# Performance work log

Hardware: AMD Instinct MI355X
Metric: run time of the kernel (lower is better)

The kernel has to match this reference:

```python
import jax, jax.numpy as jnp
import numpy as np

D = 1024
H = 16
K = 32768
EPS = 1e-5


def setup_inputs() -> dict:
    key = jax.random.key(0)
    ks = jax.random.split(key, 12)
    s = 1.0 / np.sqrt(D)
    return {
        "query": jax.random.normal(ks[0], (D,), jnp.float32),
        "neighbors": jax.random.normal(ks[1], (K, D), jnp.float32),
        # nn.MultiheadAttention params
        "in_proj_w": jax.random.uniform(ks[2], (3 * D, D), jnp.float32, -s, s),
        "in_proj_b": jnp.zeros((3 * D,), jnp.float32),
        "out_proj_w": jax.random.uniform(ks[3], (D, D), jnp.float32, -s, s),
        "out_proj_b": jnp.zeros((D,), jnp.float32),
        # FFN params
        "w1": jax.random.uniform(ks[4], (4 * D, D), jnp.float32, -s, s),
        "b1": jnp.zeros((4 * D,), jnp.float32),
        "w2": jax.random.uniform(ks[5], (D, 4 * D), jnp.float32, -s, s),
        "b2": jnp.zeros((D,), jnp.float32),
        # LayerNorm params
        "g1": jnp.ones((D,), jnp.float32),
        "be1": jnp.zeros((D,), jnp.float32),
        "g2": jnp.ones((D,), jnp.float32),
        "be2": jnp.zeros((D,), jnp.float32),
    }


def _layernorm(x, g, b):
    m = jnp.mean(x, axis=-1, keepdims=True)
    v = jnp.var(x, axis=-1, keepdims=True)
    return (x - m) * jax.lax.rsqrt(v + EPS) * g + b


def reference(query, neighbors, in_proj_w, in_proj_b, out_proj_w, out_proj_b,
              w1, b1, w2, b2, g1, be1, g2, be2):
    dh = D // H
    wq, wk, wv = in_proj_w[:D], in_proj_w[D:2 * D], in_proj_w[2 * D:]
    bq, bk, bv = in_proj_b[:D], in_proj_b[D:2 * D], in_proj_b[2 * D:]

    q = (query @ wq.T + bq).reshape(H, dh)            # [H, dh]
    k = (neighbors @ wk.T + bk).reshape(K, H, dh)     # [K, H, dh]
    v = (neighbors @ wv.T + bv).reshape(K, H, dh)

    scores = jnp.einsum('hd,khd->hk', q, k) / np.sqrt(dh)  # [H, K]
    attn = jax.nn.softmax(scores, axis=-1)
    ctx = jnp.einsum('hk,khd->hd', attn, v).reshape(D)      # [D]
    attn_out = ctx @ out_proj_w.T + out_proj_b

    x = _layernorm(query + attn_out, g1, be1)
    ffn = jax.nn.gelu(x @ w1.T + b1, approximate=False) @ w2.T + b2
    return _layernorm(x + ffn, g2, be2)
```

## Files before the change

kernel.cpp:

```cpp
#include <hip/hip_runtime.h>
#include <hip/hip_bf16.h>

#define D 1024
#define H 16
#define DH 64
#define KN 32768
#define EPS 1e-5f

__device__ __forceinline__ float wave_sum(float v){
  #pragma unroll
  for (int off = 32; off; off >>= 1) v += __shfl_xor(v, off, 64);
  return v;
}

#define GLL(gp, lp) __builtin_amdgcn_global_load_lds((const __attribute__((address_space(1))) void*)(gp), (__attribute__((address_space(3))) void*)(lp), 16, 0, 0)

__global__ __launch_bounds__(256) void g_qk(const float* __restrict__ query,
                                            const float* __restrict__ ipw, const float* __restrict__ ipb,
                                            float* __restrict__ qk, float* __restrict__ sb){
  int b = blockIdx.x, t = threadIdx.x;
  int h = b >> 2, sl = b & 3;
  int w = t >> 6, ci = t & 63;
  __shared__ float qh[DH];
  __shared__ float4 red[256];

  {
    const float4* qv = (const float4*)(query + ci*16);
    #pragma unroll 1
    for (int jj = 0; jj < 16; jj += 2){
      int j0 = h*DH + w*16 + jj;
      const float4* w0 = (const float4*)(ipw + (size_t)j0*D + ci*16);
      const float4* w1r = (const float4*)(ipw + (size_t)(j0+1)*D + ci*16);
      float a0 = 0.f, a1 = 0.f;
      #pragma unroll
      for (int c = 0; c < 4; c++){
        float4 qq = qv[c];
        float4 x0 = w0[c];
        float4 x1 = w1r[c];
        a0 += x0.x*qq.x + x0.y*qq.y + x0.z*qq.z + x0.w*qq.w;
        a1 += x1.x*qq.x + x1.y*qq.y + x1.z*qq.z + x1.w*qq.w;
      }
      a0 = wave_sum(a0);
      a1 = wave_sum(a1);
      if (ci == 0){
        qh[w*16 + jj]     = a0 + ipb[j0];
        qh[w*16 + jj + 1] = a1 + ipb[j0 + 1];
      }
    }
  }
  __syncthreads();

  if (t < DH){
    float p = qh[t] * ipb[D + h*DH + t];
    p = wave_sum(p);
    if (t == 0 && sl == 0) sb[h] = p;
  }
  float4 acc = make_float4(0.f,0.f,0.f,0.f);
  for (int jj = 0; jj < 16; jj++){
    int j = w*16 + jj;
    float4 ww = *((const float4*)(ipw + (size_t)(D + h*DH + j)*D) + sl*64 + ci);
    float qj = qh[j];
    acc.x += qj*ww.x; acc.y += qj*ww.y; acc.z += qj*ww.z; acc.w += qj*ww.w;
  }
  red[t] = acc;
  __syncthreads();
  if (w == 0){
    float4 a = red[ci], b1 = red[64+ci], c1 = red[128+ci], d1 = red[192+ci];
    float4 r = make_float4(a.x+b1.x+c1.x+d1.x, a.y+b1.y+c1.y+d1.y,
                           a.z+b1.z+c1.z+d1.z, a.w+b1.w+c1.w+d1.w);
    ((float4*)(qk + h*D))[sl*64 + ci] = r;
  }
}

__device__ __forceinline__ float bf4(float s0, float s1, float s2, float s3, int ci){
  const bool lo32 = (ci & 32) == 0;
  float za = lo32 ? s2 : s0;
  float ka = lo32 ? s0 : s2;
  float u02 = ka + __shfl_xor(za, 32, 64);
  float zb = lo32 ? s3 : s1;
  float kb = lo32 ? s1 : s3;
  float u13 = kb + __shfl_xor(zb, 32, 64);
  const bool lo16 = (ci & 16) == 0;
  float zc = lo16 ? u13 : u02;
  float kc = lo16 ? u02 : u13;
  float v = kc + __shfl_xor(zc, 16, 64);
  v += __shfl_xor(v, 8, 64);
  v += __shfl_xor(v, 4, 64);
  v += __shfl_xor(v, 2, 64);
  v += __shfl_xor(v, 1, 64);
  return v;
}

__global__ __launch_bounds__(256, 2) void g_attn(const float* __restrict__ nbr, const float* __restrict__ qk,
                       const float* __restrict__ sb, float* __restrict__ lpart,
                       float* __restrict__ part, int rows_per_blk){
  __shared__ __align__(16) float tile[2][8*D];
  const int t = threadIdx.x;
  const int w = t >> 6, ci = t & 63;
  const int wb = t & ~63;
  const int g = (ci >> 4) & 3;
  const float sbl = sb[w*4 + g];

  float qk0[16], qk1[16], qk2[16], qk3[16];
  {
    const float4* p0 = (const float4*)(qk + (w*4+0)*D);
    const float4* p1 = (const float4*)(qk + (w*4+1)*D);
    const float4* p2 = (const float4*)(qk + (w*4+2)*D);
    const float4* p3 = (const float4*)(qk + (w*4+3)*D);
    #pragma unroll
    for (int c = 0; c < 4; c++){
      float4 f;
      f = p0[c*64 + ci]; qk0[4*c]=f.x; qk0[4*c+1]=f.y; qk0[4*c+2]=f.z; qk0[4*c+3]=f.w;
      f = p1[c*64 + ci]; qk1[4*c]=f.x; qk1[4*c+1]=f.y; qk1[4*c+2]=f.z; qk1[4*c+3]=f.w;
      f = p2[c*64 + ci]; qk2[4*c]=f.x; qk2[4*c+1]=f.y; qk2[4*c+2]=f.z; qk2[4*c+3]=f.w;
      f = p3[c*64 + ci]; qk3[4*c]=f.x; qk3[4*c+1]=f.y; qk3[4*c+2]=f.z; qk3[4*c+3]=f.w;
    }
  }
  float acc0[16], acc1[16], acc2[16], acc3[16];
  #pragma unroll
  for (int i = 0; i < 16; i++){ acc0[i]=0.f; acc1[i]=0.f; acc2[i]=0.f; acc3[i]=0.f; }
  float lsum = 0.f;

  const int k0 = blockIdx.x * rows_per_blk;
  const int ntiles = rows_per_blk >> 3;
  const uint4* gb = (const uint4*)nbr;

  {
    const uint4* gsrc = gb + (size_t)k0*256;
    #pragma unroll
    for (int i = 0; i < 8; i++) GLL(gsrc + i*256 + t, &tile[0][(i*256 + wb)*4]);
  }
  __syncthreads();

  #pragma unroll 1
  for (int tl = 0; tl < ntiles; tl++){
    int cur = tl & 1;
    if (tl + 1 < ntiles){
      const uint4* gsrc = gb + (size_t)(k0 + (tl+1)*8)*256;
      #pragma unroll
      for (int i = 0; i < 8; i++) GLL(gsrc + i*256 + t, &tile[cur^1][(i*256 + wb)*4]);
    }
    __builtin_amdgcn_s_setprio(1);
    #pragma unroll 1
    for (int r = 0; r < 8; r += 2){
      const float4* rowA = (const float4*)(tile[cur]) + r*256;
      float xfA[16], xfB[16];
      float sA0=0.f,sA1=0.f,sA2=0.f,sA3=0.f;
      float sB0=0.f,sB1=0.f,sB2=0.f,sB3=0.f;
      #pragma unroll
      for (int c = 0; c < 4; c++){
        float4 a = rowA[c*64 + ci];
        xfA[4*c]=a.x; xfA[4*c+1]=a.y; xfA[4*c+2]=a.z; xfA[4*c+3]=a.w;
        sA0 += a.x*qk0[4*c] + a.y*qk0[4*c+1] + a.z*qk0[4*c+2] + a.w*qk0[4*c+3];
        sA1 += a.x*qk1[4*c] + a.y*qk1[4*c+1] + a.z*qk1[4*c+2] + a.w*qk1[4*c+3];
        sA2 += a.x*qk2[4*c] + a.y*qk2[4*c+1] + a.z*qk2[4*c+2] + a.w*qk2[4*c+3];
        sA3 += a.x*qk3[4*c] + a.y*qk3[4*c+1] + a.z*qk3[4*c+2] + a.w*qk3[4*c+3];
      }
      #pragma unroll
      for (int c = 0; c < 4; c++){
        float4 a = rowA[256 + c*64 + ci];
        xfB[4*c]=a.x; xfB[4*c+1]=a.y; xfB[4*c+2]=a.z; xfB[4*c+3]=a.w;
        sB0 += a.x*qk0[4*c] + a.y*qk0[4*c+1] + a.z*qk0[4*c+2] + a.w*qk0[4*c+3];
        sB1 += a.x*qk1[4*c] + a.y*qk1[4*c+1] + a.z*qk1[4*c+2] + a.w*qk1[4*c+3];
        sB2 += a.x*qk2[4*c] + a.y*qk2[4*c+1] + a.z*qk2[4*c+2] + a.w*qk2[4*c+3];
        sB3 += a.x*qk3[4*c] + a.y*qk3[4*c+1] + a.z*qk3[4*c+2] + a.w*qk3[4*c+3];
      }
      float vA = bf4(sA0, sA1, sA2, sA3, ci);
      float vB = bf4(sB0, sB1, sB2, sB3, ci);
      float pA = __expf((vA + sbl)*0.125f);
      float pB = __expf((vB + sbl)*0.125f);
      lsum += pA + pB;
      float pA0 = __shfl(pA, 0, 64), pA1 = __shfl(pA, 16, 64);
      float pA2 = __shfl(pA, 32, 64), pA3 = __shfl(pA, 48, 64);
      float pB0 = __shfl(pB, 0, 64), pB1 = __shfl(pB, 16, 64);
      float pB2 = __shfl(pB, 32, 64), pB3 = __shfl(pB, 48, 64);
      #pragma unroll
      for (int j = 0; j < 16; j++){
        acc0[j] += pA0*xfA[j] + pB0*xfB[j];
        acc1[j] += pA1*xfA[j] + pB1*xfB[j];
        acc2[j] += pA2*xfA[j] + pB2*xfB[j];
        acc3[j] += pA3*xfA[j] + pB3*xfB[j];
      }
    }
    __builtin_amdgcn_s_setprio(0);
    __syncthreads();
  }

  if ((ci & 15) == 0) lpart[blockIdx.x*H + w*4 + g] = lsum;
  float4* o = (float4*)(part + (size_t)blockIdx.x*(H*D) + (size_t)(w*4)*D);
  #pragma unroll
  for (int c = 0; c < 4; c++){
    o[0*256 + c*64 + ci] = make_float4(acc0[4*c], acc0[4*c+1], acc0[4*c+2], acc0[4*c+3]);
    o[1*256 + c*64 + ci] = make_float4(acc1[4*c], acc1[4*c+1], acc1[4*c+2], acc1[4*c+3]);
    o[2*256 + c*64 + ci] = make_float4(acc2[4*c], acc2[4*c+1], acc2[4*c+2], acc2[4*c+3]);
    o[3*256 + c*64 + ci] = make_float4(acc3[4*c], acc3[4*c+1], acc3[4*c+2], acc3[4*c+3]);
  }
}

__global__ __launch_bounds__(1024) void g_red(const float* __restrict__ part, const float* __restrict__ lpart,
                                              float* __restrict__ nb, float* __restrict__ lh, int nblk){
  int b = blockIdx.x, t = threadIdx.x;
  __shared__ float red[1024];
  if (b == 256){
    if (t < 256){
      int hh = t & 15, cs = t >> 4, per = nblk >> 4;
      float s = 0.f;
      for (int k = 0; k < per; k++) s += lpart[(cs*per + k)*H + hh];
      red[t] = s;
    }
    __syncthreads();
    if (t < 16){
      float a = 0.f;
      #pragma unroll
      for (int i = 0; i < 16; i++) a += red[i*16 + t];
      lh[t] = a;
    }
    return;
  }
  int o0 = b * 64;
  int oo = t & 63, cs = t >> 6;
  int per = nblk >> 4;
  float s = 0.f;
  #pragma unroll 8
  for (int k = 0; k < per; k++) s += part[(size_t)(cs*per + k)*(H*D) + o0 + oo];
  red[t] = s;
  __syncthreads();
  if (t < 64){
    float a = 0.f;
    #pragma unroll
    for (int i = 0; i < 16; i++) a += red[i*64 + t];
    nb[o0 + t] = a;
  }
}

__global__ void g_ctx(const float* __restrict__ ipw, const float* __restrict__ ipb,
                      const float* __restrict__ nb, const float* __restrict__ lh,
                      float* __restrict__ ctx){
  int j = blockIdx.x, l = threadIdx.x, h = j >> 6;
  const float4* wv = (const float4*)(ipw + (size_t)(2*D + j)*D + l*16);
  const float4* nv = (const float4*)(nb + h*D + l*16);
  float acc = 0.f;
  #pragma unroll
  for (int t = 0; t < 4; t++){
    float4 b = wv[t], n = nv[t];
    acc += b.x*n.x + b.y*n.y + b.z*n.z + b.w*n.w;
  }
  acc = wave_sum(acc);
  if (l == 0) ctx[j] = acc/lh[h] + ipb[2*D + j];
}

__global__ void g_attnout(const float* __restrict__ opw, const float* __restrict__ opb,
                          const float* __restrict__ query, const float* __restrict__ ctx,
                          float* __restrict__ xb){
  int j = blockIdx.x, l = threadIdx.x;
  const float4* wv = (const float4*)(opw + (size_t)j*D + l*16);
  const float4* cv = (const float4*)(ctx + l*16);
  float acc = 0.f;
  #pragma unroll
  for (int t = 0; t < 4; t++){
    float4 b = wv[t], c = cv[t];
    acc += b.x*c.x + b.y*c.y + b.z*c.z + b.w*c.w;
  }
  acc = wave_sum(acc);
  if (l == 0) xb[j] = query[j] + acc + opb[j];
}

__global__ __launch_bounds__(256) void g_ffn1(const float* __restrict__ w1, const float* __restrict__ b1,
                                              const float* __restrict__ xb,
                                              const float* __restrict__ g1, const float* __restrict__ be1,
                                              float* __restrict__ xln, float* __restrict__ h1){
  int t = threadIdx.x, b = blockIdx.x;
  __shared__ float xs[D];
  __shared__ float red[8];
  float4 v = ((const float4*)xb)[t];
  float s = wave_sum(v.x + v.y + v.z + v.w);
  if ((t & 63) == 0) red[t >> 6] = s;
  __syncthreads();
  float m = (red[0]+red[1]+red[2]+red[3]) * (1.0f/D);
  float4 d = make_float4(v.x-m, v.y-m, v.z-m, v.w-m);
  float s2 = wave_sum(d.x*d.x + d.y*d.y + d.z*d.z + d.w*d.w);
  if ((t & 63) == 0) red[4 + (t >> 6)] = s2;
  __syncthreads();
  float var = (red[4]+red[5]+red[6]+red[7]) * (1.0f/D);
  float rs = rsqrtf(var + EPS);
  float4 gg = ((const float4*)g1)[t], bb = ((const float4*)be1)[t];
  float4 r = make_float4(d.x*rs*gg.x + bb.x, d.y*rs*gg.y + bb.y,
                         d.z*rs*gg.z + bb.z, d.w*rs*gg.w + bb.w);
  ((float4*)xs)[t] = r;
  if (b == 0) ((float4*)xln)[t] = r;
  __syncthreads();

  int w = t >> 6, l = t & 63;
  const float4* xs4 = (const float4*)xs;
  #pragma unroll 1
  for (int rr = 0; rr < 4; rr++){
    int j = b*16 + w*4 + rr;
    const float4* wr = (const float4*)(w1 + (size_t)j*D);
    float a = 0.f;
    #pragma unroll
    for (int c = 0; c < 4; c++){
      float4 ww = wr[c*64 + l], xx = xs4[c*64 + l];
      a += ww.x*xx.x + ww.y*xx.y + ww.z*xx.z + ww.w*xx.w;
    }
    a = wave_sum(a);
    if (l == 0){
      float z = a + b1[j];
      h1[j] = 0.5f*z*(1.0f + erff(z*0.70710678118654752f));
    }
  }
}

__global__ void g_ffn2(const float* __restrict__ w2, const float* __restrict__ b2v,
                       const float* __restrict__ h1, float* __restrict__ y){
  int j = blockIdx.x, l = threadIdx.x;
  const float4* wv = (const float4*)(w2 + (size_t)j*4096 + l*64);
  const float4* hv = (const float4*)(h1 + l*64);
  float acc = 0.f;
  #pragma unroll
  for (int t = 0; t < 16; t++){
    float4 b = wv[t], hh = hv[t];
    acc += b.x*hh.x + b.y*hh.y + b.z*hh.z + b.w*hh.w;
  }
  acc = wave_sum(acc);
  if (l == 0) y[j] = acc + b2v[j];
}

__global__ __launch_bounds__(1024) void g_ln2(const float* __restrict__ xln, const float* __restrict__ y,
                                              const float* __restrict__ g, const float* __restrict__ be,
                                              float* __restrict__ out){
  int t = threadIdx.x;
  __shared__ float red[16];
  __shared__ float bc;
  float v = xln[t] + y[t];
  float s = wave_sum(v);
  if ((t & 63) == 0) red[t >> 6] = s;
  __syncthreads();
  if (t == 0){ float a = 0.f; for (int i = 0; i < 16; i++) a += red[i]; bc = a*(1.0f/D); }
  __syncthreads();
  float m = bc;
  float d = v - m;
  float s2 = wave_sum(d*d);
  if ((t & 63) == 0) red[t >> 6] = s2;
  __syncthreads();
  if (t == 0){ float a = 0.f; for (int i = 0; i < 16; i++) a += red[i]; bc = a*(1.0f/D); }
  __syncthreads();
  float rs = rsqrtf(bc + EPS);
  out[t] = d*rs*g[t] + be[t];
}

extern "C" void kernel_launch(void* const* d_in, const int* in_sizes, int n_in,
                              void* d_out, int out_size, void* d_ws, size_t ws_size,
                              hipStream_t stream) {
  const float* query = (const float*)d_in[0];
  const float* nbr   = (const float*)d_in[1];
  const float* ipw   = (const float*)d_in[2];
  const float* ipb   = (const float*)d_in[3];
  const float* opw   = (const float*)d_in[4];
  const float* opb   = (const float*)d_in[5];
  const float* w1    = (const float*)d_in[6];
  const float* b1    = (const float*)d_in[7];
  const float* w2    = (const float*)d_in[8];
  const float* b2v   = (const float*)d_in[9];
  const float* g1    = (const float*)d_in[10];
  const float* be1   = (const float*)d_in[11];
  const float* g2    = (const float*)d_in[12];
  const float* be2   = (const float*)d_in[13];

  float* ws    = (float*)d_ws;
  float* qk    = ws;
  float* sb    = qk + H*D;
  float* lh    = sb + 16;
  float* ctx   = lh + 16;
  float* xb    = ctx + D;
  float* xln   = xb + D;
  float* h1    = xln + D;
  float* y     = h1 + 4*D;
  float* nb    = y + D;
  float* lpart = nb + H*D;
  float* part  = lpart + 8192;

  size_t fixed_bytes = (size_t)(part - ws) * 4;
  int nblk = 512;
  while (nblk > 64 && fixed_bytes + (size_t)nblk*H*D*4 > ws_size) nblk >>= 1;
  int rows_per_blk = KN / nblk;

  g_qk     <<<64, 256, 0, stream>>>(query, ipw, ipb, qk, sb);
  g_attn   <<<nblk, 256, 0, stream>>>(nbr, qk, sb, lpart, part, rows_per_blk);
  g_red    <<<257, 1024, 0, stream>>>(part, lpart, nb, lh, nblk);
  g_ctx    <<<1024, 64, 0, stream>>>(ipw, ipb, nb, lh, ctx);
  g_attnout<<<1024, 64, 0, stream>>>(opw, opb, query, ctx, xb);
  g_ffn1   <<<256, 256, 0, stream>>>(w1, b1, xb, g1, be1, xln, h1);
  g_ffn2   <<<1024, 64, 0, stream>>>(w2, b2v, h1, y);
  g_ln2    <<<1, 1024, 0, stream>>>(xln, y, g2, be2, (float*)d_out);
}
```

Measured before the change: 306.9 us.

## Split attention heads across 8 waves and coalesce FFN2 weight loads

The attention kernel now launches 512 threads per block, so each wave handles 2 heads instead of 4. This halves the per-thread qk and accumulator register arrays and removes the two-row batching and the priority hints, with the aim of raising occupancy for latency hiding. The LDS tile load is spread across the 512 threads. Separately, the FFN2 kernel now reads weights and activations with a stride across lanes so the loads coalesce, instead of each lane reading a contiguous 64-float chunk. The risk is that the neighbor tile in LDS is now read by 8 waves instead of 4, doubling LDS read traffic per row.

```diff
diff --git a/kernel.cpp b/kernel.cpp
--- a/kernel.cpp
+++ b/kernel.cpp
@@ -72,53 +72,30 @@
   }
 }
 
-__device__ __forceinline__ float bf4(float s0, float s1, float s2, float s3, int ci){
-  const bool lo32 = (ci & 32) == 0;
-  float za = lo32 ? s2 : s0;
-  float ka = lo32 ? s0 : s2;
-  float u02 = ka + __shfl_xor(za, 32, 64);
-  float zb = lo32 ? s3 : s1;
-  float kb = lo32 ? s1 : s3;
-  float u13 = kb + __shfl_xor(zb, 32, 64);
-  const bool lo16 = (ci & 16) == 0;
-  float zc = lo16 ? u13 : u02;
-  float kc = lo16 ? u02 : u13;
-  float v = kc + __shfl_xor(zc, 16, 64);
-  v += __shfl_xor(v, 8, 64);
-  v += __shfl_xor(v, 4, 64);
-  v += __shfl_xor(v, 2, 64);
-  v += __shfl_xor(v, 1, 64);
-  return v;
-}
-
-__global__ __launch_bounds__(256, 2) void g_attn(const float* __restrict__ nbr, const float* __restrict__ qk,
+__global__ __launch_bounds__(512, 4) void g_attn(const float* __restrict__ nbr, const float* __restrict__ qk,
                        const float* __restrict__ sb, float* __restrict__ lpart,
                        float* __restrict__ part, int rows_per_blk){
   __shared__ __align__(16) float tile[2][8*D];
   const int t = threadIdx.x;
   const int w = t >> 6, ci = t & 63;
   const int wb = t & ~63;
-  const int g = (ci >> 4) & 3;
-  const float sbl = sb[w*4 + g];
-
-  float qk0[16], qk1[16], qk2[16], qk3[16];
+  const int g = (ci >> 5) & 1;
+  const float sbl = sb[w*2 + g];
+
+  float qk0[16], qk1[16];
   {
-    const float4* p0 = (const float4*)(qk + (w*4+0)*D);
-    const float4* p1 = (const float4*)(qk + (w*4+1)*D);
-    const float4* p2 = (const float4*)(qk + (w*4+2)*D);
-    const float4* p3 = (const float4*)(qk + (w*4+3)*D);
+    const float4* p0 = (const float4*)(qk + (w*2+0)*D);
+    const float4* p1 = (const float4*)(qk + (w*2+1)*D);
     #pragma unroll
     for (int c = 0; c < 4; c++){
       float4 f;
       f = p0[c*64 + ci]; qk0[4*c]=f.x; qk0[4*c+1]=f.y; qk0[4*c+2]=f.z; qk0[4*c+3]=f.w;
       f = p1[c*64 + ci]; qk1[4*c]=f.x; qk1[4*c+1]=f.y; qk1[4*c+2]=f.z; qk1[4*c+3]=f.w;
-      f = p2[c*64 + ci]; qk2[4*c]=f.x; qk2[4*c+1]=f.y; qk2[4*c+2]=f.z; qk2[4*c+3]=f.w;
-      f = p3[c*64 + ci]; qk3[4*c]=f.x; qk3[4*c+1]=f.y; qk3[4*c+2]=f.z; qk3[4*c+3]=f.w;
-    }
-  }
-  float acc0[16], acc1[16], acc2[16], acc3[16];
-  #pragma unroll
-  for (int i = 0; i < 16; i++){ acc0[i]=0.f; acc1[i]=0.f; acc2[i]=0.f; acc3[i]=0.f; }
+    }
+  }
+  float acc0[16], acc1[16];
+  #pragma unroll
+  for (int i = 0; i < 16; i++){ acc0[i]=0.f; acc1[i]=0.f; }
   float lsum = 0.f;
 
   const int k0 = blockIdx.x * rows_per_blk;
@@ -128,7 +105,7 @@
   {
     const uint4* gsrc = gb + (size_t)k0*256;
     #pragma unroll
-    for (int i = 0; i < 8; i++) GLL(gsrc + i*256 + t, &tile[0][(i*256 + wb)*4]);
+    for (int i = 0; i < 4; i++) GLL(gsrc + i*512 + t, &tile[0][(i*512 + wb)*4]);
   }
   __syncthreads();
 
@@ -138,62 +115,48 @@
     if (tl + 1 < ntiles){
       const uint4* gsrc = gb + (size_t)(k0 + (tl+1)*8)*256;
       #pragma unroll
-      for (int i = 0; i < 8; i++) GLL(gsrc + i*256 + t, &tile[cur^1][(i*256 + wb)*4]);
-    }
-    __builtin_amdgcn_s_setprio(1);
+      for (int i = 0; i < 4; i++) GLL(gsrc + i*512 + t, &tile[cur^1][(i*512 + wb)*4]);
+    }
     #pragma unroll 1
-    for (int r = 0; r < 8; r += 2){
-      const float4* rowA = (const float4*)(tile[cur]) + r*256;
-      float xfA[16], xfB[16];
-      float sA0=0.f,sA1=0.f,sA2=0.f,sA3=0.f;
-      float sB0=0.f,sB1=0.f,sB2=0.f,sB3=0.f;
+    for (int r = 0; r < 8; r++){
+      const float4* row4 = (const float4*)(tile[cur]) + r*256;
+      float xf[16];
+      float s0 = 0.f, s1 = 0.f;
       #pragma unroll
       for (int c = 0; c < 4; c++){
-        float4 a = rowA[c*64 + ci];
-        xfA[4*c]=a.x; xfA[4*c+1]=a.y; xfA[4*c+2]=a.z; xfA[4*c+3]=a.w;
-        sA0 += a.x*qk0[4*c] + a.y*qk0[4*c+1] + a.z*qk0[4*c+2] + a.w*qk0[4*c+3];
-        sA1 += a.x*qk1[4*c] + a.y*qk1[4*c+1] + a.z*qk1[4*c+2] + a.w*qk1[4*c+3];
-        sA2 += a.x*qk2[4*c] + a.y*qk2[4*c+1] + a.z*qk2[4*c+2] + a.w*qk2[4*c+3];
-        sA3 += a.x*qk3[4*c] + a.y*qk3[4*c+1] + a.z*qk3[4*c+2] + a.w*qk3[4*c+3];
+        float4 a = row4[c*64 + ci];
+        xf[4*c]=a.x; xf[4*c+1]=a.y; xf[4*c+2]=a.z; xf[4*c+3]=a.w;
+        s0 += a.x*qk0[4*c] + a.y*qk0[4*c+1] + a.z*qk0[4*c+2] + a.w*qk0[4*c+3];
+        s1 += a.x*qk1[4*c] + a.y*qk1[4*c+1] + a.z*qk1[4*c+2] + a.w*qk1[4*c+3];
       }
-      #pragma unroll
-      for (int c = 0; c < 4; c++){
-        float4 a = rowA[256 + c*64 + ci];
-        xfB[4*c]=a.x; xfB[4*c+1]=a.y; xfB[4*c+2]=a.z; xfB[4*c+3]=a.w;
-        sB0 += a.x*qk0[4*c] + a.y*qk0[4*c+1] + a.z*qk0[4*c+2] + a.w*qk0[4*c+3];
-        sB1 += a.x*qk1[4*c] + a.y*qk1[4*c+1] + a.z*qk1[4*c+2] + a.w*qk1[4*c+3];
-        sB2 += a.x*qk2[4*c] + a.y*qk2[4*c+1] + a.z*qk2[4*c+2] + a.w*qk2[4*c+3];
-        sB3 += a.x*qk3[4*c] + a.y*qk3[4*c+1] + a.z*qk3[4*c+2] + a.w*qk3[4*c+3];
+      bool lo = (ci & 32) == 0;
+      float z = lo ? s1 : s0;
+      float k = lo ? s0 : s1;
+      float v = k + __shfl_xor(z, 32, 64);
+      v += __shfl_xor(v, 16, 64);
+      v += __shfl_xor(v, 8, 64);
+      v += __shfl_xor(v, 4, 64);
+      v += __shfl_xor(v, 2, 64);
+      v += __shfl_xor(v, 1, 64);
+      float pv = __expf((v + sbl)*0.125f);
+      lsum += pv;
+      float pa = __shfl(pv, 0, 64);
+      float pb = __shfl(pv, 32, 64);
+      #pragma unroll
+      for (int j = 0; j < 16; j++){
+        acc0[j] += pa*xf[j];
+        acc1[j] += pb*xf[j];
       }
-      float vA = bf4(sA0, sA1, sA2, sA3, ci);
-      float vB = bf4(sB0, sB1, sB2, sB3, ci);
-      float pA = __expf((vA + sbl)*0.125f);
-      float pB = __expf((vB + sbl)*0.125f);
-      lsum += pA + pB;
-      float pA0 = __shfl(pA, 0, 64), pA1 = __shfl(pA, 16, 64);
-      float pA2 = __shfl(pA, 32, 64), pA3 = __shfl(pA, 48, 64);
-      float pB0 = __shfl(pB, 0, 64), pB1 = __shfl(pB, 16, 64);
-      float pB2 = __shfl(pB, 32, 64), pB3 = __shfl(pB, 48, 64);
-      #pragma unroll
-      for (int j = 0; j < 16; j++){
-        acc0[j] += pA0*xfA[j] + pB0*xfB[j];
-        acc1[j] += pA1*xfA[j] + pB1*xfB[j];
-        acc2[j] += pA2*xfA[j] + pB2*xfB[j];
-        acc3[j] += pA3*xfA[j] + pB3*xfB[j];
-      }
-    }
-    __builtin_amdgcn_s_setprio(0);
+    }
     __syncthreads();
   }
 
-  if ((ci & 15) == 0) lpart[blockIdx.x*H + w*4 + g] = lsum;
-  float4* o = (float4*)(part + (size_t)blockIdx.x*(H*D) + (size_t)(w*4)*D);
+  if ((ci & 31) == 0) lpart[blockIdx.x*H + w*2 + g] = lsum;
+  float4* o = (float4*)(part + (size_t)blockIdx.x*(H*D) + (size_t)(w*2)*D);
   #pragma unroll
   for (int c = 0; c < 4; c++){
-    o[0*256 + c*64 + ci] = make_float4(acc0[4*c], acc0[4*c+1], acc0[4*c+2], acc0[4*c+3]);
-    o[1*256 + c*64 + ci] = make_float4(acc1[4*c], acc1[4*c+1], acc1[4*c+2], acc1[4*c+3]);
-    o[2*256 + c*64 + ci] = make_float4(acc2[4*c], acc2[4*c+1], acc2[4*c+2], acc2[4*c+3]);
-    o[3*256 + c*64 + ci] = make_float4(acc3[4*c], acc3[4*c+1], acc3[4*c+2], acc3[4*c+3]);
+    o[c*64 + ci]       = make_float4(acc0[4*c], acc0[4*c+1], acc0[4*c+2], acc0[4*c+3]);
+    o[256 + c*64 + ci] = make_float4(acc1[4*c], acc1[4*c+1], acc1[4*c+2], acc1[4*c+3]);
   }
 }
 
@@ -313,13 +276,13 @@
 __global__ void g_ffn2(const float* __restrict__ w2, const float* __restrict__ b2v,
                        const float* __restrict__ h1, float* __restrict__ y){
   int j = blockIdx.x, l = threadIdx.x;
-  const float4* wv = (const float4*)(w2 + (size_t)j*4096 + l*64);
-  const float4* hv = (const float4*)(h1 + l*64);
+  const float4* wr = (const float4*)(w2 + (size_t)j*4096);
+  const float4* hv = (const float4*)h1;
   float acc = 0.f;
   #pragma unroll
-  for (int t = 0; t < 16; t++){
-    float4 b = wv[t], hh = hv[t];
-    acc += b.x*hh.x + b.y*hh.y + b.z*hh.z + b.w*hh.w;
+  for (int c = 0; c < 16; c++){
+    float4 ww = wr[c*64 + l], hh = hv[c*64 + l];
+    acc += ww.x*hh.x + ww.y*hh.y + ww.z*hh.z + ww.w*hh.w;
   }
   acc = wave_sum(acc);
   if (l == 0) y[j] = acc + b2v[j];
@@ -385,7 +348,7 @@
   int rows_per_blk = KN / nblk;
 
   g_qk     <<<64, 256, 0, stream>>>(query, ipw, ipb, qk, sb);
-  g_attn   <<<nblk, 256, 0, stream>>>(nbr, qk, sb, lpart, part, rows_per_blk);
+  g_attn   <<<nblk, 512, 0, stream>>>(nbr, qk, sb, lpart, part, rows_per_blk);
   g_red    <<<257, 1024, 0, stream>>>(part, lpart, nb, lh, nblk);
   g_ctx    <<<1024, 64, 0, stream>>>(ipw, ipb, nb, lh, ctx);
   g_attnout<<<1024, 64, 0, stream>>>(opw, opb, query, ctx, xb);
```

New measurement: 302.8 us. No clear change (-1.3%).
